# Performance work log

Hardware: AMD Instinct MI355X
Metric: run time of the kernel (lower is better)

## Reference

```python
import jax, jax.numpy as jnp
import numpy as np

NUM_HEAD = 8


def setup_inputs() -> dict:
    key = jax.random.key(0)
    k1, k2, k3 = jax.random.split(key, 3)
    B, C, H, W = 8, 512, 32, 32
    x = jax.random.normal(k1, (B, C, H, W), dtype=jnp.float32)
    # 1x1 conv weights stored as plain matrices (out_ch, in_ch)
    Wqkv = jax.random.normal(k2, (3 * C, C), dtype=jnp.float32) * (1.0 / np.sqrt(C))
    Wo = jax.random.normal(k3, (C, C), dtype=jnp.float32) * (1.0 / np.sqrt(C))
    bo = jnp.zeros((C,), dtype=jnp.float32)
    return {"x": x, "Wqkv": Wqkv, "Wo": Wo, "bo": bo}


def reference(x, Wqkv, Wo, bo):
    B, C, H, W = x.shape
    nh = NUM_HEAD
    d = C // nh
    S = H * W
    scale = 1.0 / np.sqrt(d)
    # 1x1 conv == channel matmul: (B,3C,H,W)
    x_ = jnp.einsum('bchw,oc->bohw', x, Wqkv)
    # reshape to (B, nh, 3d, H, W) and chunk along dim 2 (matches torch chunk order)
    qkv = x_.reshape(B, nh, 3 * d, H, W)
    q, k, v = qkv[:, :, :d], qkv[:, :, d:2 * d], qkv[:, :, 2 * d:]
    # flatten heads into batch, spatial into sequence
    q = q.reshape(B * nh, d, S).transpose(0, 2, 1) * scale  # (BH, S, d)
    k = k.reshape(B * nh, d, S)                             # (BH, d, S)
    v = v.reshape(B * nh, d, S).transpose(0, 2, 1)          # (BH, S, d)
    attn = jax.nn.softmax(jnp.matmul(q, k), axis=-1)        # (BH, S, S)
    out = jnp.matmul(attn, v)                               # (BH, S, d)
    result = out.transpose(0, 2, 1).reshape(B, C, H, W)
    # output 1x1 conv with bias + residual
    y = jnp.einsum('bchw,oc->bohw', result, Wo) + bo[None, :, None, None]
    return y + x
```

## Files before the change

kernel.cpp:

```cpp
#include <hip/hip_runtime.h>
#include <hip/hip_bf16.h>

#define C_DIM 512
#define S_DIM 1024
#define NH 8
#define HD 64

typedef __attribute__((ext_vector_type(8))) short bf16x8;
typedef __attribute__((ext_vector_type(8))) unsigned short u16x8;
typedef __attribute__((ext_vector_type(4))) unsigned short u16x4;
typedef __attribute__((ext_vector_type(4))) float f32x4;

__device__ __forceinline__ unsigned short f2b_hw(float f) {
  __hip_bfloat16 h = __float2bfloat16(f);
  return __builtin_bit_cast(unsigned short, h);
}

__device__ __forceinline__ f32x4 mfma16(bf16x8 a, bf16x8 b, f32x4 c) {
  return __builtin_amdgcn_mfma_f32_16x16x32_bf16(a, b, c, 0, 0, 0);
}

__device__ __forceinline__ void gload_lds16(const unsigned short* g, unsigned short* l) {
  __builtin_amdgcn_global_load_lds(
      (const __attribute__((address_space(1))) unsigned int*)g,
      (__attribute__((address_space(3))) unsigned int*)l, 16, 0, 0);
}

__global__ __launch_bounds__(256) void convert_w(
    const float* __restrict__ Wqkv, const float* __restrict__ Wo,
    unsigned short* __restrict__ WqkvB, unsigned short* __restrict__ WoB)
{
  const int i = blockIdx.x * 256 + threadIdx.x;
  const float* src;
  unsigned short* dst;
  int off;
  if (i < 196608) { src = Wqkv; dst = WqkvB; off = i * 4; }
  else            { src = Wo;   dst = WoB;   off = (i - 196608) * 4; }
  const float4 v = *(const float4*)(src + off);
  const u16x4 pk = {f2b_hw(v.x), f2b_hw(v.y), f2b_hw(v.z), f2b_hw(v.w)};
  *(u16x4*)(dst + off) = pk;
}

__global__ __launch_bounds__(256) void xpose_bf16(
    const float* __restrict__ x, unsigned short* __restrict__ xT)
{
  const int b = blockIdx.z, ct = blockIdx.y, st = blockIdx.x;
  const int c0 = ct * 64, s0 = st * 64;
  __shared__ float T[64][65];
  const int tr = threadIdx.x >> 4, tc4 = (threadIdx.x & 15) * 4;
#pragma unroll
  for (int rep = 0; rep < 4; ++rep) {
    const int c = rep * 16 + tr;
    *(float4*)&T[c][tc4] = *(const float4*)(x + ((size_t)(b * C_DIM + c0 + c)) * S_DIM + s0 + tc4);
  }
  __syncthreads();
#pragma unroll
  for (int rep = 0; rep < 4; ++rep) {
    const int s = rep * 16 + tr;
    const u16x4 pk = {f2b_hw(T[tc4 + 0][s]), f2b_hw(T[tc4 + 1][s]),
                      f2b_hw(T[tc4 + 2][s]), f2b_hw(T[tc4 + 3][s])};
    *(u16x4*)(xT + ((size_t)(b * S_DIM + s0 + s)) * C_DIM + c0 + tc4) = pk;
  }
}

template <int MODE>
__global__ __launch_bounds__(256) void mfma_proj(
    const unsigned short* __restrict__ A, const unsigned short* __restrict__ Bm,
    unsigned short* __restrict__ Q, unsigned short* __restrict__ K,
    unsigned short* __restrict__ Vt,
    float* __restrict__ y, const float* __restrict__ bo,
    const float* __restrict__ resid)
{
  const int b = blockIdx.z, ot = blockIdx.y, st = blockIdx.x;
  const int o0 = ot * 128, s0 = st * 128;
  const int tid = threadIdx.x;
  const int w = tid >> 6, lane = tid & 63;
  const int g = lane >> 4, j16 = lane & 15;
  const int wr = w >> 1, wc = w & 1;

  __shared__ __align__(16) unsigned short lds[2048 * 8];
  char* const Al = (char*)lds;
  char* const Bl = (char*)lds + 16384;

  f32x4 acc[4][4];
#pragma unroll
  for (int mt = 0; mt < 4; ++mt)
#pragma unroll
    for (int nt = 0; nt < 4; ++nt) {
      acc[mt][nt].x = 0.f; acc[mt][nt].y = 0.f;
      acc[mt][nt].z = 0.f; acc[mt][nt].w = 0.f;
    }

  for (int k0 = 0; k0 < C_DIM; k0 += 64) {
    __syncthreads();
#pragma unroll
    for (int it = 0; it < 8; ++it) {
      const int chunk = it * 256 + tid;
      const int cid = chunk & 1023;
      const int row = cid >> 3;
      const int colb = (cid & 7) << 4;
      const int srcb = colb ^ ((row & 7) << 4);
      const unsigned short* gp;
      if (it < 4) gp = A + (size_t)(o0 + row) * C_DIM + k0 + (srcb >> 1);
      else        gp = Bm + ((size_t)(b * S_DIM) + s0 + row) * C_DIM + k0 + (srcb >> 1);
      gload_lds16(gp, lds + (size_t)(it * 256 + w * 64) * 8);
    }
    __syncthreads();

#pragma unroll
    for (int ks = 0; ks < 2; ++ks) {
      bf16x8 af[4], bfr[4];
#pragma unroll
      for (int mt = 0; mt < 4; ++mt) {
        const int r = wr * 64 + mt * 16 + j16;
        af[mt] = __builtin_bit_cast(
            bf16x8, *(const u16x8*)(Al + r * 128 + ((ks * 64 + g * 16) ^ ((r & 7) << 4))));
      }
#pragma unroll
      for (int nt = 0; nt < 4; ++nt) {
        const int r = wc * 64 + nt * 16 + j16;
        bfr[nt] = __builtin_bit_cast(
            bf16x8, *(const u16x8*)(Bl + r * 128 + ((ks * 64 + g * 16) ^ ((r & 7) << 4))));
      }
#pragma unroll
      for (int mt = 0; mt < 4; ++mt)
#pragma unroll
        for (int nt = 0; nt < 4; ++nt)
          acc[mt][nt] = mfma16(af[mt], bfr[nt], acc[mt][nt]);
    }
  }

#pragma unroll
  for (int mt = 0; mt < 4; ++mt) {
    const int ob = o0 + wr * 64 + mt * 16 + g * 4;
    if (MODE == 0) {
      const int head = ob / 192, type = (ob % 192) >> 6, d = ob & 63;
      const int bh = b * NH + head;
#pragma unroll
      for (int nt = 0; nt < 4; ++nt) {
        const int s = s0 + wc * 64 + nt * 16 + j16;
        const f32x4 a = acc[mt][nt];
        if (type == 0) {
          const float m = 0.18033688011112042f;
          const u16x4 pk = {f2b_hw(a.x * m), f2b_hw(a.y * m), f2b_hw(a.z * m), f2b_hw(a.w * m)};
          *(u16x4*)(Q + ((size_t)bh * S_DIM + s) * HD + d) = pk;
        } else if (type == 1) {
          const u16x4 pk = {f2b_hw(a.x), f2b_hw(a.y), f2b_hw(a.z), f2b_hw(a.w)};
          *(u16x4*)(K + ((size_t)bh * S_DIM + s) * HD + d) = pk;
        } else {
#pragma unroll
          for (int q = 0; q < 4; ++q)
            Vt[((size_t)bh * HD + d + q) * S_DIM + s] = f2b_hw(a[q]);
        }
      }
    } else {
#pragma unroll
      for (int nt = 0; nt < 4; ++nt) {
        const int s = s0 + wc * 64 + nt * 16 + j16;
#pragma unroll
        for (int q = 0; q < 4; ++q) {
          const int o = ob + q;
          const size_t idx = ((size_t)(b * C_DIM + o)) * S_DIM + s;
          y[idx] = acc[mt][nt][q] + bo[o] + resid[idx];
        }
      }
    }
  }
}

__global__ __launch_bounds__(256) void attn_mfma(
    const unsigned short* __restrict__ Qg, const unsigned short* __restrict__ Kg,
    const unsigned short* __restrict__ Vg, unsigned short* __restrict__ AOt)
{
  const int bh = blockIdx.x;
  const int qb = blockIdx.y;
  const int b = bh >> 3, head = bh & 7;
  const int tid = threadIdx.x;
  const int w = tid >> 6, lane = tid & 63;
  const int g = lane >> 4, j16 = lane & 15;
  const int qw0 = qb * 128 + w * 32;

  __shared__ __align__(16) unsigned short KV[2][2][4096];

  bf16x8 qf[2][2];
#pragma unroll
  for (int nt = 0; nt < 2; ++nt)
#pragma unroll
    for (int ks = 0; ks < 2; ++ks)
      qf[nt][ks] = __builtin_bit_cast(
          bf16x8, *(const u16x8*)(Qg + ((size_t)bh * S_DIM + qw0 + nt * 16 + j16) * HD +
                                  ks * 32 + g * 8));

  auto STAGE = [&](int buf, int k0) {
#pragma unroll
    for (int it = 0; it < 2; ++it) {
      const int cid = tid + it * 256;
      const int row = cid >> 3;
      const int srcb = ((cid & 7) << 4) ^ ((row & 7) << 4);
      unsigned short* const dst = &KV[buf][0][0] + (size_t)(it * 256 + w * 64) * 8;
      gload_lds16(Kg + ((size_t)bh * S_DIM + k0 + row) * HD + (srcb >> 1), dst);
      gload_lds16(Vg + ((size_t)bh * HD + row) * S_DIM + k0 + (srcb >> 1), dst + 4096);
    }
  };

  f32x4 oacc[4][2];
#pragma unroll
  for (int mt = 0; mt < 4; ++mt)
#pragma unroll
    for (int nt = 0; nt < 2; ++nt) {
      oacc[mt][nt].x = 0.f; oacc[mt][nt].y = 0.f;
      oacc[mt][nt].z = 0.f; oacc[mt][nt].w = 0.f;
    }
  float lsum[2] = {0.f, 0.f};

  STAGE(0, 0);
  __syncthreads();

  for (int kt = 0; kt < 16; ++kt) {
    if (kt < 15) STAGE((kt + 1) & 1, (kt + 1) * 64);

    const char* const Kl = (const char*)KV + (kt & 1) * 16384;
    const char* const Vl = Kl + 8192;

    f32x4 sacc[4][2];
    __builtin_amdgcn_s_setprio(1);
#pragma unroll
    for (int mt = 0; mt < 4; ++mt) {
      const int row = mt * 16 + j16;
      const int sw = (row & 7) << 4;
#pragma unroll
      for (int ks = 0; ks < 2; ++ks) {
        const bf16x8 kf = __builtin_bit_cast(
            bf16x8, *(const u16x8*)(Kl + row * 128 + ((ks * 64 + g * 16) ^ sw)));
        if (ks == 0) {
#pragma unroll
          for (int nt = 0; nt < 2; ++nt) {
            f32x4 z; z.x = 0.f; z.y = 0.f; z.z = 0.f; z.w = 0.f;
            sacc[mt][nt] = mfma16(kf, qf[nt][0], z);
          }
        } else {
#pragma unroll
          for (int nt = 0; nt < 2; ++nt)
            sacc[mt][nt] = mfma16(kf, qf[nt][1], sacc[mt][nt]);
        }
      }
    }
    __builtin_amdgcn_s_setprio(0);

    u16x4 pf4[2][4];
#pragma unroll
    for (int mt = 0; mt < 4; ++mt)
#pragma unroll
      for (int nt = 0; nt < 2; ++nt) {
        f32x4 p;
        p.x = exp2f(sacc[mt][nt].x);
        p.y = exp2f(sacc[mt][nt].y);
        p.z = exp2f(sacc[mt][nt].z);
        p.w = exp2f(sacc[mt][nt].w);
        lsum[nt] += (p.x + p.y) + (p.z + p.w);
        pf4[nt][mt] = u16x4{f2b_hw(p.x), f2b_hw(p.y), f2b_hw(p.z), f2b_hw(p.w)};
      }

    __builtin_amdgcn_s_setprio(1);
#pragma unroll
    for (int ks = 0; ks < 2; ++ks) {
      bf16x8 pfr[2];
#pragma unroll
      for (int nt = 0; nt < 2; ++nt) {
        u16x8 t;
#pragma unroll
        for (int e = 0; e < 4; ++e) { t[e] = pf4[nt][2 * ks][e]; t[e + 4] = pf4[nt][2 * ks + 1][e]; }
        pfr[nt] = __builtin_bit_cast(bf16x8, t);
      }
#pragma unroll
      for (int mt = 0; mt < 4; ++mt) {
        const int row = mt * 16 + j16;
        const int sw = (row & 7) << 4;
        const u16x4 lo = *(const u16x4*)(Vl + row * 128 + ((ks * 64 + g * 8) ^ sw));
        const u16x4 hi = *(const u16x4*)(Vl + row * 128 + ((ks * 64 + 32 + g * 8) ^ sw));
        u16x8 t;
#pragma unroll
        for (int e = 0; e < 4; ++e) { t[e] = lo[e]; t[e + 4] = hi[e]; }
        const bf16x8 vf = __builtin_bit_cast(bf16x8, t);
#pragma unroll
        for (int nt = 0; nt < 2; ++nt)
          oacc[mt][nt] = mfma16(vf, pfr[nt], oacc[mt][nt]);
      }
    }
    __builtin_amdgcn_s_setprio(0);

    __syncthreads();
  }

#pragma unroll
  for (int nt = 0; nt < 2; ++nt) {
    lsum[nt] += __shfl_xor(lsum[nt], 16);
    lsum[nt] += __shfl_xor(lsum[nt], 32);
    lsum[nt] = 1.f / lsum[nt];
  }

#pragma unroll
  for (int mt = 0; mt < 4; ++mt)
#pragma unroll
    for (int nt = 0; nt < 2; ++nt) {
      const int q = qw0 + nt * 16 + j16;
      const f32x4 a = oacc[mt][nt];
      const float rl = lsum[nt];
      const u16x4 pk = {f2b_hw(a.x * rl), f2b_hw(a.y * rl), f2b_hw(a.z * rl), f2b_hw(a.w * rl)};
      *(u16x4*)(AOt + ((size_t)(b * S_DIM + q)) * C_DIM + head * HD + mt * 16 + g * 4) = pk;
    }
}

extern "C" void kernel_launch(void* const* d_in, const int* in_sizes, int n_in,
                              void* d_out, int out_size, void* d_ws, size_t ws_size,
                              hipStream_t stream) {
  const float* x    = (const float*)d_in[0];
  const float* Wqkv = (const float*)d_in[1];
  const float* Wo   = (const float*)d_in[2];
  const float* bo   = (const float*)d_in[3];
  float* y = (float*)d_out;

  unsigned short* WqkvB = (unsigned short*)d_ws;
  unsigned short* WoB   = WqkvB + 786432;
  unsigned short* xT    = WoB + 262144;
  unsigned short* Q     = xT + 4194304;
  unsigned short* K     = Q + 4194304;
  unsigned short* Vt    = K + 4194304;
  unsigned short* AOt   = Vt + 4194304;

  convert_w<<<dim3(1024), 256, 0, stream>>>(Wqkv, Wo, WqkvB, WoB);
  xpose_bf16<<<dim3(16, 8, 8), 256, 0, stream>>>(x, xT);
  mfma_proj<0><<<dim3(8, 12, 8), 256, 0, stream>>>(WqkvB, xT, Q, K, Vt,
                                                   nullptr, nullptr, nullptr);
  attn_mfma<<<dim3(64, 8), 256, 0, stream>>>(Q, K, Vt, AOt);
  mfma_proj<1><<<dim3(8, 4, 8), 256, 0, stream>>>(WoB, AOt, nullptr, nullptr, nullptr,
                                                  y, bo, x);
}
```

Baseline: 92.23 us.

## Merge prep kernels, fold Q scale into weights, permute V for 16-byte LDS reads

Merges the weight conversion and the x transpose into a single prep launch, saving one kernel launch. The softmax scale is folded into the Q rows of the bf16 weight matrix, so the projection epilogue no longer multiplies Q. V columns are stored in a permuted order so the attention kernel can read each V fragment with one 16-byte LDS load instead of two 8-byte loads and a repack. The permutation has to match the P fragment layout exactly, and rounding the scaled weights to bf16 changes numerics slightly.

```diff
diff --git a/kernel.cpp b/kernel.cpp
--- a/kernel.cpp
+++ b/kernel.cpp
@@ -26,40 +26,50 @@
       (__attribute__((address_space(3))) unsigned int*)l, 16, 0, 0);
 }
 
-__global__ __launch_bounds__(256) void convert_w(
-    const float* __restrict__ Wqkv, const float* __restrict__ Wo,
-    unsigned short* __restrict__ WqkvB, unsigned short* __restrict__ WoB)
+__global__ __launch_bounds__(256) void prep(
+    const float* __restrict__ x, const float* __restrict__ Wqkv,
+    const float* __restrict__ Wo,
+    unsigned short* __restrict__ WqkvB, unsigned short* __restrict__ WoB,
+    unsigned short* __restrict__ xT)
 {
-  const int i = blockIdx.x * 256 + threadIdx.x;
-  const float* src;
-  unsigned short* dst;
-  int off;
-  if (i < 196608) { src = Wqkv; dst = WqkvB; off = i * 4; }
-  else            { src = Wo;   dst = WoB;   off = (i - 196608) * 4; }
-  const float4 v = *(const float4*)(src + off);
-  const u16x4 pk = {f2b_hw(v.x), f2b_hw(v.y), f2b_hw(v.z), f2b_hw(v.w)};
-  *(u16x4*)(dst + off) = pk;
-}
-
-__global__ __launch_bounds__(256) void xpose_bf16(
-    const float* __restrict__ x, unsigned short* __restrict__ xT)
-{
-  const int b = blockIdx.z, ct = blockIdx.y, st = blockIdx.x;
-  const int c0 = ct * 64, s0 = st * 64;
   __shared__ float T[64][65];
-  const int tr = threadIdx.x >> 4, tc4 = (threadIdx.x & 15) * 4;
-#pragma unroll
-  for (int rep = 0; rep < 4; ++rep) {
-    const int c = rep * 16 + tr;
-    *(float4*)&T[c][tc4] = *(const float4*)(x + ((size_t)(b * C_DIM + c0 + c)) * S_DIM + s0 + tc4);
-  }
-  __syncthreads();
-#pragma unroll
-  for (int rep = 0; rep < 4; ++rep) {
-    const int s = rep * 16 + tr;
-    const u16x4 pk = {f2b_hw(T[tc4 + 0][s]), f2b_hw(T[tc4 + 1][s]),
-                      f2b_hw(T[tc4 + 2][s]), f2b_hw(T[tc4 + 3][s])};
-    *(u16x4*)(xT + ((size_t)(b * S_DIM + s0 + s)) * C_DIM + c0 + tc4) = pk;
+  const int bid = blockIdx.x;
+  if (bid < 1024) {
+    const int i = bid * 256 + threadIdx.x;
+    const float* src;
+    unsigned short* dst;
+    int off;
+    float mul = 1.0f;
+    if (i < 196608) {
+      src = Wqkv; dst = WqkvB; off = i * 4;
+      const int o = off >> 9;
+      if ((o % 192) < 64) mul = 0.18033688011112042f;
+    } else {
+      src = Wo; dst = WoB; off = (i - 196608) * 4;
+    }
+    const float4 v = *(const float4*)(src + off);
+    const u16x4 pk = {f2b_hw(v.x * mul), f2b_hw(v.y * mul),
+                      f2b_hw(v.z * mul), f2b_hw(v.w * mul)};
+    *(u16x4*)(dst + off) = pk;
+  } else {
+    const int idx = bid - 1024;
+    const int st = idx & 15, ct = (idx >> 4) & 7, b = idx >> 7;
+    const int c0 = ct * 64, s0 = st * 64;
+    const int tr = threadIdx.x >> 4, tc4 = (threadIdx.x & 15) * 4;
+#pragma unroll
+    for (int rep = 0; rep < 4; ++rep) {
+      const int c = rep * 16 + tr;
+      *(float4*)&T[c][tc4] =
+          *(const float4*)(x + ((size_t)(b * C_DIM + c0 + c)) * S_DIM + s0 + tc4);
+    }
+    __syncthreads();
+#pragma unroll
+    for (int rep = 0; rep < 4; ++rep) {
+      const int s = rep * 16 + tr;
+      const u16x4 pk = {f2b_hw(T[tc4 + 0][s]), f2b_hw(T[tc4 + 1][s]),
+                        f2b_hw(T[tc4 + 2][s]), f2b_hw(T[tc4 + 3][s])};
+      *(u16x4*)(xT + ((size_t)(b * S_DIM + s0 + s)) * C_DIM + c0 + tc4) = pk;
+    }
   }
 }
 
@@ -136,21 +146,25 @@
     if (MODE == 0) {
       const int head = ob / 192, type = (ob % 192) >> 6, d = ob & 63;
       const int bh = b * NH + head;
-#pragma unroll
-      for (int nt = 0; nt < 4; ++nt) {
-        const int s = s0 + wc * 64 + nt * 16 + j16;
-        const f32x4 a = acc[mt][nt];
-        if (type == 0) {
-          const float m = 0.18033688011112042f;
-          const u16x4 pk = {f2b_hw(a.x * m), f2b_hw(a.y * m), f2b_hw(a.z * m), f2b_hw(a.w * m)};
-          *(u16x4*)(Q + ((size_t)bh * S_DIM + s) * HD + d) = pk;
-        } else if (type == 1) {
+      if (type < 2) {
+        unsigned short* const dst = (type == 0) ? Q : K;
+#pragma unroll
+        for (int nt = 0; nt < 4; ++nt) {
+          const int s = s0 + wc * 64 + nt * 16 + j16;
+          const f32x4 a = acc[mt][nt];
           const u16x4 pk = {f2b_hw(a.x), f2b_hw(a.y), f2b_hw(a.z), f2b_hw(a.w)};
-          *(u16x4*)(K + ((size_t)bh * S_DIM + s) * HD + d) = pk;
-        } else {
+          *(u16x4*)(dst + ((size_t)bh * S_DIM + s) * HD + d) = pk;
+        }
+      } else {
+#pragma unroll
+        for (int nt = 0; nt < 4; ++nt) {
+          const int spos = nt * 16 + j16;
+          const int p = (spos & 35) | ((spos & 12) << 1) | ((spos & 16) >> 2);
+          const size_t col = (size_t)(s0 + wc * 64 + p);
+          const f32x4 a = acc[mt][nt];
 #pragma unroll
           for (int q = 0; q < 4; ++q)
-            Vt[((size_t)bh * HD + d + q) * S_DIM + s] = f2b_hw(a[q]);
+            Vt[((size_t)bh * HD + d + q) * S_DIM + col] = f2b_hw(a[q]);
         }
       }
     } else {
@@ -266,22 +280,16 @@
     for (int ks = 0; ks < 2; ++ks) {
       bf16x8 pfr[2];
 #pragma unroll
-      for (int nt = 0; nt < 2; ++nt) {
-        u16x8 t;
-#pragma unroll
-        for (int e = 0; e < 4; ++e) { t[e] = pf4[nt][2 * ks][e]; t[e + 4] = pf4[nt][2 * ks + 1][e]; }
-        pfr[nt] = __builtin_bit_cast(bf16x8, t);
-      }
+      for (int nt = 0; nt < 2; ++nt)
+        pfr[nt] = __builtin_bit_cast(
+            bf16x8, __builtin_shufflevector(pf4[nt][2 * ks], pf4[nt][2 * ks + 1],
+                                            0, 1, 2, 3, 4, 5, 6, 7));
 #pragma unroll
       for (int mt = 0; mt < 4; ++mt) {
         const int row = mt * 16 + j16;
         const int sw = (row & 7) << 4;
-        const u16x4 lo = *(const u16x4*)(Vl + row * 128 + ((ks * 64 + g * 8) ^ sw));
-        const u16x4 hi = *(const u16x4*)(Vl + row * 128 + ((ks * 64 + 32 + g * 8) ^ sw));
-        u16x8 t;
-#pragma unroll
-        for (int e = 0; e < 4; ++e) { t[e] = lo[e]; t[e + 4] = hi[e]; }
-        const bf16x8 vf = __builtin_bit_cast(bf16x8, t);
+        const bf16x8 vf = __builtin_bit_cast(
+            bf16x8, *(const u16x8*)(Vl + row * 128 + ((ks * 64 + g * 16) ^ sw)));
 #pragma unroll
         for (int nt = 0; nt < 2; ++nt)
           oacc[mt][nt] = mfma16(vf, pfr[nt], oacc[mt][nt]);
@@ -328,8 +336,7 @@
   unsigned short* Vt    = K + 4194304;
   unsigned short* AOt   = Vt + 4194304;
 
-  convert_w<<<dim3(1024), 256, 0, stream>>>(Wqkv, Wo, WqkvB, WoB);
-  xpose_bf16<<<dim3(16, 8, 8), 256, 0, stream>>>(x, xT);
+  prep<<<dim3(2048), 256, 0, stream>>>(x, Wqkv, Wo, WqkvB, WoB, xT);
   mfma_proj<0><<<dim3(8, 12, 8), 256, 0, stream>>>(WqkvB, xT, Q, K, Vt,
                                                    nullptr, nullptr, nullptr);
   attn_mfma<<<dim3(64, 8), 256, 0, stream>>>(Q, K, Vt, AOt);
```

Result: faster. 83.87 us (-9.1%).
